# Kernel optimization log

Hardware: AMD Instinct MI355X
Metric: run time of the kernel (lower is better)

Reference implementation:

```python
import jax, jax.numpy as jnp
import numpy as np

N = 100000      # nodes
E = 1250000     # edges
DIN = 128       # input_feature_dim
H = 64          # hidden_feature_dim
C = 16          # num_classes
BN_EPS = 1e-5


def _linear_init(key, fin, fout):
    # torch.nn.Linear default: U(-1/sqrt(fin), 1/sqrt(fin)); stored as [fin, fout] for x @ W
    s = 1.0 / np.sqrt(fin)
    kw, kb = jax.random.split(key)
    w = jax.random.uniform(kw, (fin, fout), jnp.float32, -s, s)
    b = jax.random.uniform(kb, (fout,), jnp.float32, -s, s)
    return w, b


def setup_inputs() -> dict:
    key = jax.random.key(0)
    ks = jax.random.split(key, 16)
    inp = {}
    inp["x"] = jax.random.normal(ks[0], (N, DIN), jnp.float32)
    src = jax.random.randint(ks[1], (E,), 0, N)
    dst = jax.random.randint(ks[2], (E,), 0, N)
    inp["edge_index"] = jnp.stack([src, dst]).astype(jnp.int64)
    inp["fc1_w"], inp["fc1_b"] = _linear_init(ks[3], DIN, H)
    dims = [(H, H), (H, H), (H, C)]
    for i, (fi, fo) in enumerate(dims):
        w, b = _linear_init(ks[4 + i], fi, fo)
        inp[f"conv{i}_w"] = w
        inp[f"conv{i}_b"] = b
        inp[f"bn{i}_g"] = jnp.ones((fo,), jnp.float32)
        inp[f"bn{i}_b"] = jnp.zeros((fo,), jnp.float32)
    inp["fc2_w"], inp["fc2_b"] = _linear_init(ks[7], C, C)
    return inp


def gcn_conv(h, w, b, src, dst, n):
    # PyG GCNConv: linear transform, add self-loops, symmetric normalization,
    # scatter-add messages from src into dst, then add bias.
    h = h @ w                                   # [N, out]
    loops = jnp.arange(n)
    s = jnp.concatenate([src, loops])           # [E+N]
    d = jnp.concatenate([dst, loops])
    deg = jax.ops.segment_sum(jnp.ones(s.shape[0], h.dtype), d, num_segments=n)
    dinv = jnp.where(deg > 0, jax.lax.rsqrt(deg), 0.0)
    norm = dinv[s] * dinv[d]                    # [E+N]
    msg = h[s] * norm[:, None]                  # [E+N, out] gather + scale
    out = jax.ops.segment_sum(msg, d, num_segments=n)
    return out + b


def batch_norm(x, gamma, beta):
    # BatchNorm1d in training mode: biased batch statistics over nodes
    mu = x.mean(axis=0)
    var = x.var(axis=0)
    return (x - mu) * jax.lax.rsqrt(var + BN_EPS) * gamma + beta


def reference(x, edge_index, fc1_w, fc1_b,
              conv0_w, conv0_b, bn0_g, bn0_b,
              conv1_w, conv1_b, bn1_g, bn1_b,
              conv2_w, conv2_b, bn2_g, bn2_b,
              fc2_w, fc2_b):
    src, dst = edge_index[0], edge_index[1]
    n = x.shape[0]
    h = jax.nn.relu(x @ fc1_w + fc1_b)
    layers = [(conv0_w, conv0_b, bn0_g, bn0_b),
              (conv1_w, conv1_b, bn1_g, bn1_b),
              (conv2_w, conv2_b, bn2_g, bn2_b)]
    for w, b, g, be in layers:
        h = jax.nn.relu(batch_norm(gcn_conv(h, w, b, src, dst, n), g, be))
    h = h @ fc2_w + fc2_b
    return jax.nn.log_softmax(h, axis=1)
```

## Files before the change

kernel.cpp:

```cpp
#include <hip/hip_runtime.h>

#define BN_EPS 1e-5f

typedef unsigned int uint32;

__device__ __forceinline__ void fma4(float4& a, float s, const float4& w) {
    a.x = fmaf(s, w.x, a.x); a.y = fmaf(s, w.y, a.y);
    a.z = fmaf(s, w.z, a.z); a.w = fmaf(s, w.w, a.w);
}

__device__ __forceinline__ float blo(uint32 p) { return __uint_as_float(p << 16); }
__device__ __forceinline__ float bhi(uint32 p) { return __uint_as_float(p & 0xFFFF0000u); }
__device__ __forceinline__ uint32 f2bf1(float f) {
    uint32 u = __float_as_uint(f);
    return (u + 0x7FFFu + ((u >> 16) & 1u)) >> 16;
}
__device__ __forceinline__ uint32 packbf(float a, float b) { return f2bf1(a) | (f2bf1(b) << 16); }


__global__ __launch_bounds__(256) void k_deg_count(const int* __restrict__ dst, int* deg, int e) {
    int i = blockIdx.x * 256 + threadIdx.x;
    if (i < e) atomicAdd(&deg[dst[i]], 1);
}


__global__ __launch_bounds__(256) void k_scan1(const int* __restrict__ deg, int* __restrict__ off,
                                               int* __restrict__ bsum, float* __restrict__ dinv, int n) {
    __shared__ int sh[256];
    int i = blockIdx.x * 256 + threadIdx.x;
    int v = (i < n) ? deg[i] : 0;
    if (i < n) dinv[i] = rsqrtf((float)v + 1.0f);
    sh[threadIdx.x] = v;
    __syncthreads();
    #pragma unroll
    for (int d = 1; d < 256; d <<= 1) {
        int t = (threadIdx.x >= d) ? sh[threadIdx.x - d] : 0;
        __syncthreads();
        sh[threadIdx.x] += t;
        __syncthreads();
    }
    if (i < n) off[i] = sh[threadIdx.x] - v;
    if (threadIdx.x == 255) bsum[blockIdx.x] = sh[255];
}

__global__ __launch_bounds__(512) void k_scan2(int* bsum, int nb) {
    __shared__ int sh[512];
    int v = (threadIdx.x < nb) ? bsum[threadIdx.x] : 0;
    sh[threadIdx.x] = v;
    __syncthreads();
    #pragma unroll
    for (int d = 1; d < 512; d <<= 1) {
        int t = (threadIdx.x >= d) ? sh[threadIdx.x - d] : 0;
        __syncthreads();
        sh[threadIdx.x] += t;
        __syncthreads();
    }
    if (threadIdx.x < nb) bsum[threadIdx.x] = sh[threadIdx.x] - v;
}

__global__ __launch_bounds__(256) void k_scan3(int* __restrict__ off, const int* __restrict__ bsum,
                                               int* __restrict__ cnt, int n, int e) {
    int i = blockIdx.x * 256 + threadIdx.x;
    if (i < n) { off[i] += bsum[blockIdx.x]; cnt[i] = 0; }
    if (i == 0) off[n] = e;
}

__global__ __launch_bounds__(256) void k_fill(const int* __restrict__ src, const int* __restrict__ dst,
                                              const int* __restrict__ off, int* __restrict__ cnt,
                                              int* __restrict__ esrc, int e) {
    int i = blockIdx.x * 256 + threadIdx.x;
    if (i < e) {
        int d = dst[i];
        int slot = off[d] + atomicAdd(&cnt[d], 1);
        esrc[slot] = src[i];
    }
}


template<int FIN, int FOUT, bool RELU, bool BIAS, bool BNIN, bool DSCALE, bool OBF>
__global__ __launch_bounds__(256) void k_linear(const float* __restrict__ X, const float* __restrict__ W,
                                                const float* __restrict__ bias, void* __restrict__ Yv,
                                                const float* __restrict__ S, const float* __restrict__ bng,
                                                const float* __restrict__ bnb, const float* __restrict__ dinv,
                                                float inv_n, int n) {
    constexpr int KC = 64;
    constexpr int TX = FOUT / 4;
    constexpr int TY = 256 / TX;
    constexpr int RQ = (FOUT == 64) ? 4 : 2;
    constexpr int TILE_R = TY * RQ;
    constexpr int LDX = KC + 4;
    constexpr int LDW = FOUT + 4;
    __shared__ float Xs[TILE_R][LDX];
    __shared__ float Ws[KC][LDW];
    __shared__ float scs[BNIN ? FIN : 4], sfs[BNIN ? FIN : 4];

    const int tx = threadIdx.x % TX;
    const int ty = threadIdx.x / TX;

    if (BNIN) {
        for (int c = threadIdx.x; c < FIN; c += 256) {
            float mu = S[c] * inv_n;
            float var = S[FIN + c] * inv_n - mu * mu;
            float is = rsqrtf(var + BN_EPS) * bng[c];
            scs[c] = is;
            sfs[c] = bnb[c] - mu * is;
        }
        __syncthreads();
    }

    float4 bb = make_float4(0.f, 0.f, 0.f, 0.f);
    if (BIAS) bb = *(const float4*)(bias + tx * 4);

    for (int r0 = blockIdx.x * TILE_R; r0 < n; r0 += gridDim.x * TILE_R) {
        float4 acc[RQ];
        #pragma unroll
        for (int q = 0; q < RQ; ++q) acc[q] = bb;

        for (int kc = 0; kc < FIN; kc += KC) {
            __syncthreads();
            for (int idx = threadIdx.x; idx < TILE_R * (KC / 4); idx += 256) {
                int rr = idx / (KC / 4), k4 = idx % (KC / 4);
                int row = r0 + rr;
                float4 v = make_float4(0.f, 0.f, 0.f, 0.f);
                if (row < n) v = *(const float4*)(X + (size_t)row * FIN + kc + 4 * k4);
                if (BNIN) {
                    int c = kc + 4 * k4;
                    v.x = fmaxf(fmaf(v.x, scs[c+0], sfs[c+0]), 0.f);
                    v.y = fmaxf(fmaf(v.y, scs[c+1], sfs[c+1]), 0.f);
                    v.z = fmaxf(fmaf(v.z, scs[c+2], sfs[c+2]), 0.f);
                    v.w = fmaxf(fmaf(v.w, scs[c+3], sfs[c+3]), 0.f);
                }
                *(float4*)(&Xs[rr][4 * k4]) = v;
            }
            for (int idx = threadIdx.x; idx < KC * (FOUT / 4); idx += 256) {
                int kk = idx / (FOUT / 4), c4 = idx % (FOUT / 4);
                *(float4*)(&Ws[kk][4 * c4]) = *(const float4*)(W + (size_t)(kc + kk) * FOUT + 4 * c4);
            }
            __syncthreads();

            #pragma unroll 4
            for (int k4 = 0; k4 < KC / 4; ++k4) {
                float4 w0 = *(const float4*)(&Ws[4*k4+0][tx*4]);
                float4 w1 = *(const float4*)(&Ws[4*k4+1][tx*4]);
                float4 w2 = *(const float4*)(&Ws[4*k4+2][tx*4]);
                float4 w3 = *(const float4*)(&Ws[4*k4+3][tx*4]);
                #pragma unroll
                for (int q = 0; q < RQ; ++q) {
                    float4 xv = *(const float4*)(&Xs[ty*RQ+q][4*k4]);
                    fma4(acc[q], xv.x, w0);
                    fma4(acc[q], xv.y, w1);
                    fma4(acc[q], xv.z, w2);
                    fma4(acc[q], xv.w, w3);
                }
            }
        }

        #pragma unroll
        for (int q = 0; q < RQ; ++q) {
            int row = r0 + ty * RQ + q;
            if (row < n) {
                float4 v = acc[q];
                if (RELU) {
                    v.x = fmaxf(v.x, 0.f); v.y = fmaxf(v.y, 0.f);
                    v.z = fmaxf(v.z, 0.f); v.w = fmaxf(v.w, 0.f);
                }
                if (DSCALE) {
                    float dv = dinv[row];
                    v.x *= dv; v.y *= dv; v.z *= dv; v.w *= dv;
                }
                if (OBF) {
                    uint2 pk;
                    pk.x = packbf(v.x, v.y);
                    pk.y = packbf(v.z, v.w);
                    ((uint2*)Yv)[(size_t)row * (FOUT / 4) + tx] = pk;
                } else {
                    *(float4*)((float*)Yv + (size_t)row * FOUT + tx * 4) = v;
                }
            }
        }
    }
}


__global__ __launch_bounds__(256) void k_accum64bf(const uint32* __restrict__ Tb, const int* __restrict__ esrc,
                                                   const int* __restrict__ off, const float* __restrict__ dinv,
                                                   const float* __restrict__ bias, float* __restrict__ Z,
                                                   float* __restrict__ S, int n, int npw) {
    __shared__ uint32 ring[4][2][256];
    __shared__ float sA[4][64], sB[4][64];

    const int lane = threadIdx.x & 63;
    const int wid  = threadIdx.x >> 6;
    const int rsub = lane >> 3;
    const int csub = lane & 7;
    const int cidx = lane >> 1;
    const int chal = lane & 1;
    const float bcol = bias[lane];

    float s1 = 0.f, s2 = 0.f;

    const int gw = blockIdx.x * 4 + wid;
    const int d0 = gw * npw;

    if (d0 < n) {
        const int d1 = min(d0 + npw, n);
        const int e0 = off[d0];
        const int e1 = off[d1];
        const int nt = (e1 - e0 + 7) >> 3;

        uint32* slot0 = &ring[wid][0][0];
        uint32* slot1 = &ring[wid][1][0];

        int d = d0;
        int nxt = off[d + 1];
        uint32 selfp = Tb[(size_t)d * 32 + cidx];
        float  dv    = dinv[d];
        float  part  = 0.f;
        int    ec    = e0;

        auto tload = [&](int t) -> uint4 {
            int ei = min(e0 + t * 8 + rsub, e1 - 1);
            int s = esrc[ei];
            return ((const uint4*)Tb)[(size_t)s * 8 + csub];
        };

        uint4 B0, B1, B2;
        if (nt > 0) B0 = tload(0);
        if (nt > 1) B1 = tload(1);
        if (nt > 2) B2 = tload(2);

        for (int t = 0; t < nt; ++t) {
            uint32* sl = (t & 1) ? slot1 : slot0;
            uint4 cur = (t % 3 == 0) ? B0 : (t % 3 == 1) ? B1 : B2;
            *(uint4*)(sl + lane * 4) = cur;
            if (t + 3 < nt) {
                if (t % 3 == 0) B0 = tload(t + 3);
                else if (t % 3 == 1) B1 = tload(t + 3);
                else B2 = tload(t + 3);
            }
            int rend = min(8, e1 - (e0 + t * 8));
            for (int r = 0; r < rend; ++r) {
                while (ec == nxt) {
                    float sv = chal ? bhi(selfp) : blo(selfp);
                    float z = fmaf(part + sv, dv, bcol);
                    Z[(size_t)d * 64 + lane] = z;
                    s1 += z; s2 += z * z;
                    part = 0.f;
                    ++d;
                    nxt = off[d + 1];
                    selfp = Tb[(size_t)d * 32 + cidx];
                    dv = dinv[d];
                }
                uint32 p = sl[r * 32 + cidx];
                part += chal ? bhi(p) : blo(p);
                ++ec;
            }
        }
        while (d < d1) {
            float sv = chal ? bhi(selfp) : blo(selfp);
            float z = fmaf(part + sv, dv, bcol);
            Z[(size_t)d * 64 + lane] = z;
            s1 += z; s2 += z * z;
            part = 0.f;
            ++d;
            if (d < d1) {
                selfp = Tb[(size_t)d * 32 + cidx];
                dv = dinv[d];
            }
        }
    }

    sA[wid][lane] = s1;
    sB[wid][lane] = s2;
    __syncthreads();
    if (threadIdx.x < 64) {
        float t1 = 0.f, t2 = 0.f;
        #pragma unroll
        for (int w = 0; w < 4; ++w) { t1 += sA[w][threadIdx.x]; t2 += sB[w][threadIdx.x]; }
        atomicAdd(&S[threadIdx.x], t1);
        atomicAdd(&S[64 + threadIdx.x], t2);
    }
}


__global__ __launch_bounds__(256) void k_accum16bf(const uint2* __restrict__ Tb2, const int* __restrict__ esrc,
                                                   const int* __restrict__ off, const float* __restrict__ dinv,
                                                   const float* __restrict__ bias, float* __restrict__ Z,
                                                   float* __restrict__ S, int n) {
    const int lane = threadIdx.x & 63;
    const int wid  = threadIdx.x >> 6;
    const int lp   = lane & 3;
    const int es   = lane >> 2;
    const float4 bb = *(const float4*)(bias + 4 * lp);
    float st1[4] = {0.f,0.f,0.f,0.f}, st2[4] = {0.f,0.f,0.f,0.f};
    const uint2 z2 = make_uint2(0u, 0u);

    for (int dp = blockIdx.x * 4 + wid; 2 * dp < n; dp += gridDim.x * 4) {
        const int dA = 2 * dp, dB = 2 * dp + 1;
        const int oA0 = off[dA], oA1 = off[dA + 1];
        const int oB0 = oA1;
        const int oB1 = (dB < n) ? off[dB + 1] : oA1;

        float aA0=0.f, aA1=0.f, aA2=0.f, aA3=0.f;
        float aB0=0.f, aB1=0.f, aB2=0.f, aB3=0.f;
        int bA = oA0, bB = oB0;
        while (bA < oA1 || bB < oB1) {
            if (bA < oA1) {
                int i0 = bA + es;
                int s0 = (i0 < oA1) ? esrc[i0] : -1;
                uint2 p0 = (s0 >= 0) ? Tb2[(size_t)s0 * 4 + lp] : z2;
                aA0 += blo(p0.x); aA1 += bhi(p0.x); aA2 += blo(p0.y); aA3 += bhi(p0.y);
            }
            if (bB < oB1) {
                int i0 = bB + es;
                int s0 = (i0 < oB1) ? esrc[i0] : -1;
                uint2 p0 = (s0 >= 0) ? Tb2[(size_t)s0 * 4 + lp] : z2;
                aB0 += blo(p0.x); aB1 += bhi(p0.x); aB2 += blo(p0.y); aB3 += bhi(p0.y);
            }
            bA += 16; bB += 16;
        }

        #pragma unroll
        for (int sh = 4; sh <= 32; sh <<= 1) {
            aA0 += __shfl_xor(aA0, sh); aA1 += __shfl_xor(aA1, sh);
            aA2 += __shfl_xor(aA2, sh); aA3 += __shfl_xor(aA3, sh);
            aB0 += __shfl_xor(aB0, sh); aB1 += __shfl_xor(aB1, sh);
            aB2 += __shfl_xor(aB2, sh); aB3 += __shfl_xor(aB3, sh);
        }

        if (es == 0) {
            uint2 ps = Tb2[(size_t)dA * 4 + lp];
            float dv = dinv[dA];
            float4 zz;
            zz.x = fmaf(aA0 + blo(ps.x), dv, bb.x);
            zz.y = fmaf(aA1 + bhi(ps.x), dv, bb.y);
            zz.z = fmaf(aA2 + blo(ps.y), dv, bb.z);
            zz.w = fmaf(aA3 + bhi(ps.y), dv, bb.w);
            *(float4*)(Z + (size_t)dA * 16 + 4 * lp) = zz;
            st1[0] += zz.x; st2[0] += zz.x * zz.x;
            st1[1] += zz.y; st2[1] += zz.y * zz.y;
            st1[2] += zz.z; st2[2] += zz.z * zz.z;
            st1[3] += zz.w; st2[3] += zz.w * zz.w;
            if (dB < n) {
                uint2 pb = Tb2[(size_t)dB * 4 + lp];
                float dvB = dinv[dB];
                float4 zb;
                zb.x = fmaf(aB0 + blo(pb.x), dvB, bb.x);
                zb.y = fmaf(aB1 + bhi(pb.x), dvB, bb.y);
                zb.z = fmaf(aB2 + blo(pb.y), dvB, bb.z);
                zb.w = fmaf(aB3 + bhi(pb.y), dvB, bb.w);
                *(float4*)(Z + (size_t)dB * 16 + 4 * lp) = zb;
                st1[0] += zb.x; st2[0] += zb.x * zb.x;
                st1[1] += zb.y; st2[1] += zb.y * zb.y;
                st1[2] += zb.z; st2[2] += zb.z * zb.z;
                st1[3] += zb.w; st2[3] += zb.w * zb.w;
            }
        }
    }

    __shared__ float sh1[4][16], sh2[4][16];
    if (es == 0) {
        *(float4*)(&sh1[wid][4 * lp]) = make_float4(st1[0], st1[1], st1[2], st1[3]);
        *(float4*)(&sh2[wid][4 * lp]) = make_float4(st2[0], st2[1], st2[2], st2[3]);
    }
    __syncthreads();
    if (threadIdx.x < 16) {
        float t1 = 0.f, t2 = 0.f;
        #pragma unroll
        for (int w = 0; w < 4; ++w) { t1 += sh1[w][threadIdx.x]; t2 += sh2[w][threadIdx.x]; }
        atomicAdd(&S[threadIdx.x], t1);
        atomicAdd(&S[16 + threadIdx.x], t2);
    }
}


__global__ __launch_bounds__(256) void k_fc2_lsm(const float* __restrict__ Hin, const float* __restrict__ W,
                                                 const float* __restrict__ bias, const float* __restrict__ S,
                                                 const float* __restrict__ bng, const float* __restrict__ bnb,
                                                 float inv_n, float* __restrict__ out, int n) {
    __shared__ float Ws[256];
    __shared__ float bs[16], sc[16], sf[16];
    Ws[threadIdx.x] = W[threadIdx.x];
    if (threadIdx.x < 16) {
        int c = threadIdx.x;
        bs[c] = bias[c];
        float mu = S[c] * inv_n;
        float var = S[16 + c] * inv_n - mu * mu;
        float is = rsqrtf(var + BN_EPS) * bng[c];
        sc[c] = is;
        sf[c] = bnb[c] - mu * is;
    }
    __syncthreads();
    for (int row = blockIdx.x * 256 + threadIdx.x; row < n; row += gridDim.x * 256) {
        float h[16];
        const float4* hp = (const float4*)(Hin + (size_t)row * 16);
        #pragma unroll
        for (int q = 0; q < 4; ++q) {
            float4 h4 = hp[q];
            h[q*4+0] = h4.x; h[q*4+1] = h4.y; h[q*4+2] = h4.z; h[q*4+3] = h4.w;
        }
        #pragma unroll
        for (int k = 0; k < 16; ++k) h[k] = fmaxf(fmaf(h[k], sc[k], sf[k]), 0.0f);
        float o[16];
        #pragma unroll
        for (int c = 0; c < 16; ++c) {
            float acc = bs[c];
            #pragma unroll
            for (int k = 0; k < 16; ++k) acc += h[k] * Ws[k * 16 + c];
            o[c] = acc;
        }
        float m = o[0];
        #pragma unroll
        for (int c = 1; c < 16; ++c) m = fmaxf(m, o[c]);
        float ssum = 0.f;
        #pragma unroll
        for (int c = 0; c < 16; ++c) ssum += expf(o[c] - m);
        float lse = m + logf(ssum);
        float4* op = (float4*)(out + (size_t)row * 16);
        #pragma unroll
        for (int q = 0; q < 4; ++q) {
            float4 w4;
            w4.x = o[q*4+0] - lse; w4.y = o[q*4+1] - lse;
            w4.z = o[q*4+2] - lse; w4.w = o[q*4+3] - lse;
            op[q] = w4;
        }
    }
}


extern "C" void kernel_launch(void* const* d_in, const int* in_sizes, int n_in,
                              void* d_out, int out_size, void* d_ws, size_t ws_size,
                              hipStream_t stream) {
    const float* x      = (const float*)d_in[0];
    const int*   ei     = (const int*)d_in[1];
    const float* fc1_w  = (const float*)d_in[2];
    const float* fc1_b  = (const float*)d_in[3];
    const float* conv_w[3] = { (const float*)d_in[4],  (const float*)d_in[8],  (const float*)d_in[12] };
    const float* conv_b[3] = { (const float*)d_in[5],  (const float*)d_in[9],  (const float*)d_in[13] };
    const float* bn_g[3]   = { (const float*)d_in[6],  (const float*)d_in[10], (const float*)d_in[14] };
    const float* bn_b[3]   = { (const float*)d_in[7],  (const float*)d_in[11], (const float*)d_in[15] };
    const float* fc2_w  = (const float*)d_in[16];
    const float* fc2_b  = (const float*)d_in[17];

    const int n = in_sizes[0] / 128;
    const int e = in_sizes[1] / 2;
    const int* src = ei;
    const int* dst = ei + e;
    const float inv_n = 1.0f / (float)n;

    float*  A    = (float*)d_ws;
    float*  Bf   = A + (size_t)n * 64;
    uint32* Bb   = (uint32*)Bf;
    uint2*  Bb2  = (uint2*)Bf;
    float*  dinv = Bf + (size_t)n * 64;
    int*    deg  = (int*)(dinv + n);
    int*    off  = deg + n;
    int*    esrc = off + n + 1;
    float*  stats = (float*)(esrc + e);
    int*    bsum = (int*)(stats + 384);

    const int gN  = (n + 255) / 256;
    const int gE  = (e + 255) / 256;
    const int gAcc = 2048;
    const int nwaves = gAcc * 4;
    const int npw = (n + nwaves - 1) / nwaves;
    const int gLin64 = (n + 63) / 64;
    const int gLin128 = (n + 127) / 128;

    float* st[3] = { stats, stats + 128, stats + 256 };

    hipMemsetAsync(deg, 0, (size_t)n * sizeof(int), stream);
    hipMemsetAsync(stats, 0, 384 * sizeof(float), stream);
    k_deg_count<<<gE, 256, 0, stream>>>(dst, deg, e);
    k_scan1<<<gN, 256, 0, stream>>>(deg, off, bsum, dinv, n);
    k_scan2<<<1, 512, 0, stream>>>(bsum, gN);
    k_scan3<<<gN, 256, 0, stream>>>(off, bsum, deg , n, e);
    k_fill<<<gE, 256, 0, stream>>>(src, dst, off, deg , esrc, e);

    k_linear<128, 64, true, true, false, false, false><<<gLin64, 256, 0, stream>>>(
        x, fc1_w, fc1_b, A, nullptr, nullptr, nullptr, nullptr, 0.f, n);

    k_linear<64, 64, false, false, false, true, true><<<gLin64, 256, 0, stream>>>(
        A, conv_w[0], nullptr, Bb, nullptr, nullptr, nullptr, dinv, 0.f, n);
    k_accum64bf<<<gAcc, 256, 0, stream>>>(Bb, esrc, off, dinv, conv_b[0], A, st[0], n, npw);

    k_linear<64, 64, false, false, true, true, true><<<gLin64, 256, 0, stream>>>(
        A, conv_w[1], nullptr, Bb, st[0], bn_g[0], bn_b[0], dinv, inv_n, n);
    k_accum64bf<<<gAcc, 256, 0, stream>>>(Bb, esrc, off, dinv, conv_b[1], A, st[1], n, npw);

    k_linear<64, 16, false, false, true, true, true><<<gLin128, 256, 0, stream>>>(
        A, conv_w[2], nullptr, Bb2, st[1], bn_g[1], bn_b[1], dinv, inv_n, n);
    k_accum16bf<<<gAcc, 256, 0, stream>>>(Bb2, esrc, off, dinv, conv_b[2], A, st[2], n);

    k_fc2_lsm<<<gLin64, 256, 0, stream>>>(A, fc2_w, fc2_b, st[2], bn_g[2], bn_b[2], inv_n, (float*)d_out, n);
}
```

Measured before the change: 502.2 us.

## Balance accumulation waves by edge count and enlarge linear row tiles

The 64-wide accumulation kernel now gives each wave an equal share of edges, using a binary search over the CSR offsets to find its node range, instead of a fixed number of nodes per wave. The aim is to even out load imbalance from the skewed degree distribution. The FOUT=64 linear kernels process 8 row groups per thread, so 128-row tiles and fewer blocks, which raises per-thread work and register use. The workspace is reordered so one memset clears both the degree array and the stats, removing one launch. fc2 now launches with the 128-row grid; whether that matches its internal tiling is not visible.

```diff
diff --git a/kernel.cpp b/kernel.cpp
--- a/kernel.cpp
+++ b/kernel.cpp
@@ -86,7 +86,7 @@
     constexpr int KC = 64;
     constexpr int TX = FOUT / 4;
     constexpr int TY = 256 / TX;
-    constexpr int RQ = (FOUT == 64) ? 4 : 2;
+    constexpr int RQ = (FOUT == 64) ? 8 : 2;
     constexpr int TILE_R = TY * RQ;
     constexpr int LDX = KC + 4;
     constexpr int LDW = FOUT + 4;
@@ -185,7 +185,7 @@
 __global__ __launch_bounds__(256) void k_accum64bf(const uint32* __restrict__ Tb, const int* __restrict__ esrc,
                                                    const int* __restrict__ off, const float* __restrict__ dinv,
                                                    const float* __restrict__ bias, float* __restrict__ Z,
-                                                   float* __restrict__ S, int n, int npw) {
+                                                   float* __restrict__ S, int n, int e) {
     __shared__ uint32 ring[4][2][256];
     __shared__ float sA[4][64], sB[4][64];
 
@@ -200,10 +200,22 @@
     float s1 = 0.f, s2 = 0.f;
 
     const int gw = blockIdx.x * 4 + wid;
-    const int d0 = gw * npw;
-
-    if (d0 < n) {
-        const int d1 = min(d0 + npw, n);
+    const int NW = gridDim.x * 4;
+    const int eS = (int)((long long)gw * e / NW);
+    const int eE = (int)((long long)(gw + 1) * e / NW);
+
+    int lo = 0, hi = n;
+    while (lo < hi) { int mid = (lo + hi) >> 1; if (off[mid] < eS) lo = mid + 1; else hi = mid; }
+    const int d0 = lo;
+    int d1;
+    if (gw == NW - 1) d1 = n;
+    else {
+        lo = d0; hi = n;
+        while (lo < hi) { int mid = (lo + hi) >> 1; if (off[mid] < eE) lo = mid + 1; else hi = mid; }
+        d1 = lo;
+    }
+
+    if (d0 < d1) {
         const int e0 = off[d0];
         const int e1 = off[d1];
         const int nt = (e1 - e0 + 7) >> 3;
@@ -454,43 +466,39 @@
     uint2*  Bb2  = (uint2*)Bf;
     float*  dinv = Bf + (size_t)n * 64;
     int*    deg  = (int*)(dinv + n);
-    int*    off  = deg + n;
+    float*  stats = (float*)(deg + n);
+    int*    off  = (int*)(stats + 384);
     int*    esrc = off + n + 1;
-    float*  stats = (float*)(esrc + e);
-    int*    bsum = (int*)(stats + 384);
+    int*    bsum = esrc + e;
 
     const int gN  = (n + 255) / 256;
     const int gE  = (e + 255) / 256;
     const int gAcc = 2048;
-    const int nwaves = gAcc * 4;
-    const int npw = (n + nwaves - 1) / nwaves;
-    const int gLin64 = (n + 63) / 64;
-    const int gLin128 = (n + 127) / 128;
+    const int gLin = (n + 127) / 128;
 
     float* st[3] = { stats, stats + 128, stats + 256 };
 
-    hipMemsetAsync(deg, 0, (size_t)n * sizeof(int), stream);
-    hipMemsetAsync(stats, 0, 384 * sizeof(float), stream);
+    hipMemsetAsync(deg, 0, ((size_t)n + 384) * sizeof(int), stream);
     k_deg_count<<<gE, 256, 0, stream>>>(dst, deg, e);
     k_scan1<<<gN, 256, 0, stream>>>(deg, off, bsum, dinv, n);
     k_scan2<<<1, 512, 0, stream>>>(bsum, gN);
     k_scan3<<<gN, 256, 0, stream>>>(off, bsum, deg , n, e);
     k_fill<<<gE, 256, 0, stream>>>(src, dst, off, deg , esrc, e);
 
-    k_linear<128, 64, true, true, false, false, false><<<gLin64, 256, 0, stream>>>(
+    k_linear<128, 64, true, true, false, false, false><<<gLin, 256, 0, stream>>>(
         x, fc1_w, fc1_b, A, nullptr, nullptr, nullptr, nullptr, 0.f, n);
 
-    k_linear<64, 64, false, false, false, true, true><<<gLin64, 256, 0, stream>>>(
+    k_linear<64, 64, false, false, false, true, true><<<gLin, 256, 0, stream>>>(
         A, conv_w[0], nullptr, Bb, nullptr, nullptr, nullptr, dinv, 0.f, n);
-    k_accum64bf<<<gAcc, 256, 0, stream>>>(Bb, esrc, off, dinv, conv_b[0], A, st[0], n, npw);
-
-    k_linear<64, 64, false, false, true, true, true><<<gLin64, 256, 0, stream>>>(
+    k_accum64bf<<<gAcc, 256, 0, stream>>>(Bb, esrc, off, dinv, conv_b[0], A, st[0], n, e);
+
+    k_linear<64, 64, false, false, true, true, true><<<gLin, 256, 0, stream>>>(
         A, conv_w[1], nullptr, Bb, st[0], bn_g[0], bn_b[0], dinv, inv_n, n);
-    k_accum64bf<<<gAcc, 256, 0, stream>>>(Bb, esrc, off, dinv, conv_b[1], A, st[1], n, npw);
-
-    k_linear<64, 16, false, false, true, true, true><<<gLin128, 256, 0, stream>>>(
+    k_accum64bf<<<gAcc, 256, 0, stream>>>(Bb, esrc, off, dinv, conv_b[1], A, st[1], n, e);
+
+    k_linear<64, 16, false, false, true, true, true><<<gLin, 256, 0, stream>>>(
         A, conv_w[2], nullptr, Bb2, st[1], bn_g[1], bn_b[1], dinv, inv_n, n);
     k_accum16bf<<<gAcc, 256, 0, stream>>>(Bb2, esrc, off, dinv, conv_b[2], A, st[2], n);
 
-    k_fc2_lsm<<<gLin64, 256, 0, stream>>>(A, fc2_w, fc2_b, st[2], bn_g[2], bn_b[2], inv_n, (float*)d_out, n);
-}
+    k_fc2_lsm<<<gLin, 256, 0, stream>>>(A, fc2_w, fc2_b, st[2], bn_g[2], bn_b[2], inv_n, (float*)d_out, n);
+}
```

After: 475.2 us. 5.4% less time.
